# Performance work log

Hardware: AMD Instinct MI355X
Metric: run time of the kernel (lower is better)

The kernel has to match this reference:

```python
import jax, jax.numpy as jnp
import numpy as np

EPS = 1e-5


def _bn(h, g, b):
    # training-mode batch norm over the point dimension
    m = jnp.mean(h, axis=0)
    v = jnp.mean(jnp.square(h), axis=0) - jnp.square(m)
    return g * (h - m) * jax.lax.rsqrt(v + EPS) + b


def _convtr2(x, w):
    # generative transpose conv, stride 2: each point spawns 8 children. w: [8, Cin, Cout]
    n = x.shape[0]
    return jnp.einsum('nc,kcd->nkd', x, w).reshape(n * 8, w.shape[-1])


def _conv3(x, idx, mask, w):
    # 3^3 stride-1 sparse conv via kernel-map gather + per-offset GEMM, accumulated with scan.
    # idx, mask: [27, N]; w: [27, Cin, Cout]
    acc0 = jnp.zeros((idx.shape[1], w.shape[-1]), x.dtype)

    def step(acc, kin):
        i_k, m_k, w_k = kin
        return acc + (x[i_k] * m_k[:, None]) @ w_k, None

    out, _ = jax.lax.scan(step, acc0, (idx, mask, w))
    return out


def setup_inputs() -> dict:
    key = jax.random.key(0)
    ks = jax.random.split(key, 16)
    N0, N1, N2 = 8000, 64000, 512000
    s = lambda k, shape, fan: jax.random.normal(k, shape, jnp.float32) * (1.0 / np.sqrt(fan))
    return {
        'x': jax.random.normal(ks[0], (N0, 128), jnp.float32),
        'w_tr1': s(ks[1], (8, 128, 96), 128),
        'g1': jnp.ones((96,), jnp.float32), 'b1': jnp.zeros((96,), jnp.float32),
        'idx1': jax.random.randint(ks[2], (27, N1), 0, N1, jnp.int32),
        'mask1': (jax.random.uniform(ks[3], (27, N1)) < 0.7).astype(jnp.float32),
        'w_c1': s(ks[4], (27, 96, 64), 27 * 96),
        'g2': jnp.ones((64,), jnp.float32), 'b2': jnp.zeros((64,), jnp.float32),
        'w_tr2': s(ks[5], (8, 64, 64), 64),
        'g3': jnp.ones((64,), jnp.float32), 'b3': jnp.zeros((64,), jnp.float32),
        'idx2': jax.random.randint(ks[6], (27, N2), 0, N2, jnp.int32),
        'mask2': (jax.random.uniform(ks[7], (27, N2)) < 0.7).astype(jnp.float32),
        'w_c2': s(ks[8], (27, 64, 32), 27 * 64),
        'g4': jnp.ones((32,), jnp.float32), 'b4': jnp.zeros((32,), jnp.float32),
        'w_dec': s(ks[9], (32, 96), 32),
        'g5': jnp.ones((96,), jnp.float32), 'b5': jnp.zeros((96,), jnp.float32),
    }


def reference(x, w_tr1, g1, b1, idx1, mask1, w_c1, g2, b2,
              w_tr2, g3, b3, idx2, mask2, w_c2, g4, b4, w_dec, g5, b5):
    relu = jax.nn.relu
    h = relu(_bn(_convtr2(x, w_tr1), g1, b1))            # [8*N0, 96]
    h = relu(_bn(_conv3(h, idx1, mask1, w_c1), g2, b2))  # [N1, 64]
    h = relu(_bn(_convtr2(h, w_tr2), g3, b3))            # [N2, 64]
    h = relu(_bn(_conv3(h, idx2, mask2, w_c2), g4, b4))  # [N2, 32]
    intensity_res = jnp.mean(h, axis=1, keepdims=True)   # mean_me: feature-dim mean
    remi2seg = relu(_bn(h @ w_dec, g5, b5))              # [N2, 96]
    return intensity_res, remi2seg
```

## Files before the change

### kernel.cpp

```cpp
#include <hip/hip_runtime.h>
#include <hip/hip_bf16.h>


#define EPSF 1e-5f
#define N2 512000

typedef __attribute__((ext_vector_type(8))) short short8v;
typedef __attribute__((ext_vector_type(4))) short short4v;
typedef __attribute__((ext_vector_type(4))) float f32x4;

__device__ __forceinline__ float bf2f(short u) {
  return __uint_as_float(((unsigned int)(unsigned short)u) << 16);
}
__device__ __forceinline__ short f2bf(float f) {
  __hip_bfloat16 h = __float2bfloat16(f);
  return *(short*)&h;
}

__global__ __launch_bounds__(256) void wconvA_k(
    const float* __restrict__ wc1, const float* __restrict__ wc2,
    const float* __restrict__ wt1, const float* __restrict__ wt2,
    const float* __restrict__ x,
    ushort* __restrict__ o_wc1, ushort* __restrict__ o_wc2,
    ushort* __restrict__ o_wt1, ushort* __restrict__ o_wt2,
    ushort* __restrict__ o_xb) {
  const int i = blockIdx.x * 256 + threadIdx.x;
  if (i < 165888) {
    int k = i / 6144, r = i % 6144, c = r / 64, d = r % 64;
    o_wc1[(k * 64 + d) * 96 + c] = (ushort)f2bf(wc1[i]);
  } else if (i < 221184) {
    int j = i - 165888;
    int k = j / 2048, r = j % 2048, c = r / 32, d = r % 32;
    o_wc2[(k * 32 + d) * 64 + c] = (ushort)f2bf(wc2[j]);
  } else if (i < 319488) {
    int j = i - 221184;
    int k = j / 12288, r = j % 12288, c = r / 96, d = r % 96;
    o_wt1[(k * 96 + d) * 128 + c] = (ushort)f2bf(wt1[j]);
  } else if (i < 352256) {
    int j = i - 319488;
    int k = j / 4096, r = j % 4096, c = r / 64, d = r % 64;
    o_wt2[(k * 64 + d) * 64 + c] = (ushort)f2bf(wt2[j]);
  } else if (i < 1376256) {
    int j = i - 352256;
    o_xb[j] = (ushort)f2bf(x[j]);
  }
}

__global__ __launch_bounds__(256) void wconvB_k(const float* __restrict__ wdec,
                                                ushort* __restrict__ o_wd) {
  const int i = blockIdx.x * 256 + threadIdx.x;
  if (i < 3072) {
    int c = i / 96, d = i % 96;
    o_wd[d * 32 + c] = (ushort)f2bf(wdec[i]);
  }
}

template <int CIN, int COUT, int NK, int WPB>
__global__ __launch_bounds__(WPB * 64) void convtrm_k(const ushort* __restrict__ xb,
                                                      const ushort* __restrict__ wtb,
                                                      ushort* __restrict__ yb,
                                                      float* __restrict__ st, int N) {
  constexpr int KS = CIN / 32;
  constexpr int NT = COUT / 16;
  const int t = threadIdx.x, wid = t >> 6, lane = t & 63;
  const int r16 = lane & 15, g = lane >> 4, co = g * 8;
  const int base = (blockIdx.x * WPB + wid) * 32;

  short8v A[2][KS];
#pragma unroll
  for (int m = 0; m < 2; ++m) {
    const ushort* rp = xb + (size_t)(base + m * 16 + r16) * CIN + co;
#pragma unroll
    for (int s = 0; s < KS; ++s) A[m][s] = *(const short8v*)(rp + s * 32);
  }
  float s_l[NT], q_l[NT];
#pragma unroll
  for (int n = 0; n < NT; ++n) { s_l[n] = 0.f; q_l[n] = 0.f; }

#pragma unroll 1
  for (int k = 0; k < NK; ++k) {
    f32x4 acc[2][NT];
#pragma unroll
    for (int m = 0; m < 2; ++m)
#pragma unroll
      for (int n = 0; n < NT; ++n) acc[m][n] = (f32x4)0.f;
    const ushort* wb = wtb + ((size_t)k * COUT + r16) * CIN + co;
#pragma unroll
    for (int n = 0; n < NT; ++n)
#pragma unroll
      for (int s = 0; s < KS; ++s) {
        short8v bv = *(const short8v*)(wb + n * 16 * CIN + s * 32);
        acc[0][n] = __builtin_amdgcn_mfma_f32_16x16x32_bf16(A[0][s], bv, acc[0][n], 0, 0, 0);
        acc[1][n] = __builtin_amdgcn_mfma_f32_16x16x32_bf16(A[1][s], bv, acc[1][n], 0, 0, 0);
      }
#pragma unroll
    for (int m = 0; m < 2; ++m)
#pragma unroll
      for (int n = 0; n < NT; ++n)
#pragma unroll
        for (int j = 0; j < 4; ++j) {
          float v = acc[m][n][j];
          yb[((size_t)(base + m * 16 + g * 4 + j) * NK + k) * COUT + n * 16 + r16] =
              (ushort)f2bf(v);
          s_l[n] += v; q_l[n] += v * v;
        }
  }
  __shared__ float sl[2 * COUT];
  for (int i = t; i < 2 * COUT; i += WPB * 64) sl[i] = 0.f;
  __syncthreads();
#pragma unroll
  for (int n = 0; n < NT; ++n) {
    atomicAdd(&sl[n * 16 + r16], s_l[n]);
    atomicAdd(&sl[COUT + n * 16 + r16], q_l[n]);
  }
  __syncthreads();
  for (int i = t; i < 2 * COUT; i += WPB * 64) atomicAdd(&st[i], sl[i]);
}

template <int CIN, int COUT, int MT>
__global__ __launch_bounds__(256) void conv3m_k(const ushort* __restrict__ hb,
                                                const int* __restrict__ idx,
                                                const float* __restrict__ mask,
                                                const ushort* __restrict__ wtb,
                                                ushort* __restrict__ yb,
                                                float* __restrict__ st, int N) {
  constexpr int KS = CIN / 32;
  constexpr int NT = COUT / 16;
  const int t = threadIdx.x, wid = t >> 6, lane = t & 63;
  const int r16 = lane & 15, g = lane >> 4, co = g * 8;
  const int base = (blockIdx.x * 4 + wid) * (MT * 16);

  f32x4 acc[MT][NT];
#pragma unroll
  for (int m = 0; m < MT; ++m)
#pragma unroll
    for (int n = 0; n < NT; ++n) acc[m][n] = (f32x4)0.f;

  int pn[MT];
#pragma unroll
  for (int m = 0; m < MT; ++m) pn[m] = base + m * 16 + r16;

  short8v A0[MT][KS], A1[MT][KS];

#define GATH(A, kk)                                                         \
  {                                                                         \
    const size_t kN = (size_t)(kk) * N;                                     \
    _Pragma("unroll") for (int m = 0; m < MT; ++m) {                        \
      const float mm = mask[kN + pn[m]];                                    \
      const int ii = idx[kN + pn[m]];                                       \
      const ushort* rp = hb + (size_t)ii * CIN + co;                        \
      _Pragma("unroll") for (int s = 0; s < KS; ++s) {                      \
        short8v v = (short8v)0;                                             \
        if (mm != 0.f) v = *(const short8v*)(rp + s * 32);                  \
        A[m][s] = v;                                                        \
      }                                                                     \
    }                                                                       \
  }

#define MMA(A, kk)                                                          \
  {                                                                         \
    const ushort* wb = wtb + ((size_t)(kk) * COUT + r16) * CIN + co;        \
    _Pragma("unroll") for (int n = 0; n < NT; ++n)                          \
        _Pragma("unroll") for (int s = 0; s < KS; ++s) {                    \
      short8v bv = *(const short8v*)(wb + n * 16 * CIN + s * 32);           \
      _Pragma("unroll") for (int m = 0; m < MT; ++m)                        \
          acc[m][n] = __builtin_amdgcn_mfma_f32_16x16x32_bf16(              \
              A[m][s], bv, acc[m][n], 0, 0, 0);                             \
    }                                                                       \
  }

  GATH(A0, 0)
#pragma unroll 1
  for (int k2 = 0; k2 < 13; ++k2) {
    GATH(A1, 2 * k2 + 1)
    MMA(A0, 2 * k2)
    GATH(A0, 2 * k2 + 2)
    MMA(A1, 2 * k2 + 1)
  }
  MMA(A0, 26)
#undef GATH
#undef MMA

  float s_l[NT], q_l[NT];
#pragma unroll
  for (int n = 0; n < NT; ++n) { s_l[n] = 0.f; q_l[n] = 0.f; }
#pragma unroll
  for (int m = 0; m < MT; ++m)
#pragma unroll
    for (int n = 0; n < NT; ++n)
#pragma unroll
      for (int j = 0; j < 4; ++j) {
        float v = acc[m][n][j];
        yb[(size_t)(base + m * 16 + g * 4 + j) * COUT + n * 16 + r16] = (ushort)f2bf(v);
        s_l[n] += v; q_l[n] += v * v;
      }
  __shared__ float sl[2 * COUT];
  if (t < 2 * COUT) sl[t] = 0.f;
  __syncthreads();
#pragma unroll
  for (int n = 0; n < NT; ++n) {
    atomicAdd(&sl[n * 16 + r16], s_l[n]);
    atomicAdd(&sl[COUT + n * 16 + r16], q_l[n]);
  }
  __syncthreads();
  if (t < 2 * COUT) atomicAdd(&st[t], sl[t]);
}

template <int C>
__global__ __launch_bounds__(256) void bn_bb_k(const ushort* __restrict__ in,
                                               ushort* __restrict__ out, int N,
                                               const float* __restrict__ st,
                                               const float* __restrict__ g,
                                               const float* __restrict__ b) {
  __shared__ float scs[C], bis[C];
  const int t = threadIdx.x;
  if (t < C) {
    const float invN = 1.f / (float)N;
    float m = st[t] * invN;
    float var = st[C + t] * invN - m * m;
    float rs = rsqrtf(var + EPSF);
    scs[t] = g[t] * rs;
    bis[t] = b[t] - m * g[t] * rs;
  }
  __syncthreads();
  const long total8 = (long)N * C / 8;
  for (long i = (long)blockIdx.x * 256 + t; i < total8; i += (long)gridDim.x * 256) {
    const int c0 = (int)((8 * i) % C);
    short8v v = *(const short8v*)(in + 8 * i);
    short8v o;
#pragma unroll
    for (int j = 0; j < 8; ++j) {
      float f = bf2f(v[j]);
      o[j] = f2bf(fmaxf(0.f, fmaf(f, scs[c0 + j], bis[c0 + j])));
    }
    *(short8v*)(out + 8 * i) = o;
  }
}

__global__ __launch_bounds__(256) void kint2_k(const ushort* __restrict__ y4b,
                                               float* __restrict__ inten,
                                               const float* __restrict__ st4,
                                               const float* __restrict__ g4,
                                               const float* __restrict__ b4,
                                               ushort* __restrict__ h4b) {
  __shared__ float sc[32], bi[32];
  const int t = threadIdx.x;
  if (t < 32) {
    const float invN = 1.f / (float)N2;
    float m = st4[t] * invN;
    float v = st4[32 + t] * invN - m * m;
    float rs = rsqrtf(v + EPSF);
    sc[t] = g4[t] * rs;
    bi[t] = b4[t] - m * g4[t] * rs;
  }
  __syncthreads();
  const int r = blockIdx.x * 256 + t;
  const ushort* yr = y4b + (size_t)r * 32;
  ushort* hr = h4b + (size_t)r * 32;
  float sum = 0.f;
#pragma unroll
  for (int q = 0; q < 4; ++q) {
    short8v v = *(const short8v*)(yr + 8 * q);
    short8v o;
#pragma unroll
    for (int j = 0; j < 8; ++j) {
      int c = 8 * q + j;
      float h = fmaxf(0.f, fmaf(bf2f(v[j]), sc[c], bi[c]));
      sum += h;
      o[j] = f2bf(h);
    }
    *(short8v*)(hr + 8 * q) = o;
  }
  inten[r] = sum * (1.f / 32.f);
}

__global__ __launch_bounds__(256) void kM2_k(const ushort* __restrict__ h4b,
                                             float* __restrict__ Mg,
                                             float* __restrict__ csum) {
  __shared__ float Mb[1024];
  __shared__ float Sb[32];
  const int t = threadIdx.x;
  for (int i = t; i < 1024; i += 256) Mb[i] = 0.f;
  if (t < 32) Sb[t] = 0.f;
  __syncthreads();
  const int wave = t >> 6, lane = t & 63;
  const int ci = (lane >> 3) * 4, cj = (lane & 7) * 4;
  float macc[16];
  float scl[4];
#pragma unroll
  for (int a = 0; a < 16; ++a) macc[a] = 0.f;
#pragma unroll
  for (int a = 0; a < 4; ++a) scl[a] = 0.f;
  const int base = blockIdx.x * 1000 + wave * 250;
  for (int r = 0; r < 250; ++r) {
    const ushort* yr = h4b + (size_t)(base + r) * 32;
    short4v u = *(const short4v*)(yr + ci);
    short4v w = *(const short4v*)(yr + cj);
    float hu[4], hv[4];
#pragma unroll
    for (int a = 0; a < 4; ++a) { hu[a] = bf2f(u[a]); hv[a] = bf2f(w[a]); }
#pragma unroll
    for (int a = 0; a < 4; ++a)
#pragma unroll
      for (int q = 0; q < 4; ++q) macc[a * 4 + q] = fmaf(hu[a], hv[q], macc[a * 4 + q]);
#pragma unroll
    for (int q = 0; q < 4; ++q) scl[q] += hv[q];
  }
#pragma unroll
  for (int a = 0; a < 4; ++a)
#pragma unroll
    for (int q = 0; q < 4; ++q) atomicAdd(&Mb[(ci + a) * 32 + cj + q], macc[a * 4 + q]);
  if ((lane >> 3) == 0) {
#pragma unroll
    for (int q = 0; q < 4; ++q) atomicAdd(&Sb[cj + q], scl[q]);
  }
  __syncthreads();
  for (int i = t; i < 1024; i += 256) atomicAdd(&Mg[i], Mb[i]);
  if (t < 32) atomicAdd(&csum[t], Sb[t]);
}

__global__ __launch_bounds__(128) void kstat5_k(const float* __restrict__ colsum_g,
                                                const float* __restrict__ Mg,
                                                const float* __restrict__ wd,
                                                const float* __restrict__ g5,
                                                const float* __restrict__ b5,
                                                float* __restrict__ sc5g,
                                                float* __restrict__ bi5g) {
  __shared__ float wl[3072], Ml[1024], csl[32];
  const int t = threadIdx.x;
  for (int i = t * 4; i < 3072; i += 512)
    *(float4*)&wl[i] = *(const float4*)&wd[i];
  for (int i = t; i < 1024; i += 128) Ml[i] = Mg[i];
  if (t < 32) csl[t] = colsum_g[t];
  __syncthreads();
  if (t < 96) {
    const float invN = 1.f / (float)N2;
    float mean = 0.f;
#pragma unroll
    for (int c = 0; c < 32; ++c) mean = fmaf(csl[c], wl[c * 96 + t], mean);
    mean *= invN;
    float q = 0.f;
    for (int c1 = 0; c1 < 32; ++c1) {
      float tmp = 0.f;
#pragma unroll
      for (int c2 = 0; c2 < 32; ++c2) tmp = fmaf(Ml[c1 * 32 + c2], wl[c2 * 96 + t], tmp);
      q = fmaf(wl[c1 * 96 + t], tmp, q);
    }
    float var = q * invN - mean * mean;
    float rs = rsqrtf(var + EPSF);
    float sc = g5[t] * rs;
    sc5g[t] = sc;
    bi5g[t] = b5[t] - mean * sc;
  }
}

__global__ __launch_bounds__(256) void kfinal2_k(const ushort* __restrict__ h4b,
                                                 const ushort* __restrict__ wdT,
                                                 const float* __restrict__ sc5g,
                                                 const float* __restrict__ bi5g,
                                                 float* __restrict__ outR) {
  const int t = threadIdx.x, wid = t >> 6, lane = t & 63;
  const int r16 = lane & 15, g = lane >> 4, co = g * 8;
  const int base = (blockIdx.x * 4 + wid) * 32;

  short8v a[2];
#pragma unroll
  for (int m = 0; m < 2; ++m)
    a[m] = *(const short8v*)(h4b + (size_t)(base + m * 16 + r16) * 32 + co);

  f32x4 acc[2][6];
#pragma unroll
  for (int m = 0; m < 2; ++m)
#pragma unroll
    for (int n = 0; n < 6; ++n) acc[m][n] = (f32x4)0.f;
#pragma unroll
  for (int n = 0; n < 6; ++n) {
    short8v bv = *(const short8v*)(wdT + (size_t)(n * 16 + r16) * 32 + co);
    acc[0][n] = __builtin_amdgcn_mfma_f32_16x16x32_bf16(a[0], bv, acc[0][n], 0, 0, 0);
    acc[1][n] = __builtin_amdgcn_mfma_f32_16x16x32_bf16(a[1], bv, acc[1][n], 0, 0, 0);
  }
#pragma unroll
  for (int n = 0; n < 6; ++n) {
    const int col = n * 16 + r16;
    const float sc = sc5g[col], bi = bi5g[col];
#pragma unroll
    for (int m = 0; m < 2; ++m)
#pragma unroll
      for (int j = 0; j < 4; ++j)
        outR[(size_t)(base + m * 16 + g * 4 + j) * 96 + col] =
            fmaxf(0.f, fmaf(acc[m][n][j], sc, bi));
  }
}

extern "C" void kernel_launch(void* const* d_in, const int* in_sizes, int n_in,
                              void* d_out, int out_size, void* d_ws, size_t ws_size,
                              hipStream_t stream) {
  const float* x     = (const float*)d_in[0];
  const float* w_tr1 = (const float*)d_in[1];
  const float* g1    = (const float*)d_in[2];
  const float* b1    = (const float*)d_in[3];
  const int*   idx1  = (const int*)d_in[4];
  const float* mask1 = (const float*)d_in[5];
  const float* w_c1  = (const float*)d_in[6];
  const float* g2    = (const float*)d_in[7];
  const float* b2    = (const float*)d_in[8];
  const float* w_tr2 = (const float*)d_in[9];
  const float* g3    = (const float*)d_in[10];
  const float* b3    = (const float*)d_in[11];
  const int*   idx2  = (const int*)d_in[12];
  const float* mask2 = (const float*)d_in[13];
  const float* w_c2  = (const float*)d_in[14];
  const float* g4    = (const float*)d_in[15];
  const float* b4    = (const float*)d_in[16];
  const float* w_dec = (const float*)d_in[17];
  const float* g5    = (const float*)d_in[18];
  const float* b5    = (const float*)d_in[19];

  float* outF  = (float*)d_out;
  float* inten = outF;
  float* R     = outF + 512000;

  ushort* y1b = (ushort*)R;
  ushort* h1b = (ushort*)(R + 3200000);
  ushort* y2b = (ushort*)(R + 6400000);
  ushort* h2b = (ushort*)(R + 8500000);
  ushort* y3b = (ushort*)(R + 16384000);
  ushort* h3b = (ushort*)R;
  ushort* y4b = (ushort*)(R + 32800000);
  ushort* xb  = (ushort*)(R + 41100000);

  float* iw  = inten;
  float* st1 = iw + 0;
  float* st2 = iw + 192;
  float* st3 = iw + 320;
  ushort* w1T  = (ushort*)(iw + 448);
  ushort* w2T  = (ushort*)(iw + 83392);
  ushort* wt1T = (ushort*)(iw + 111040);
  ushort* wt2T = (ushort*)(iw + 160192);

  float* xw   = (float*)d_in[0];
  float* st4  = xw + 0;
  float* csum = xw + 64;
  float* Mg   = xw + 96;
  float* sc5g = xw + 1120;
  float* bi5g = xw + 1216;
  ushort* wdT = (ushort*)(xw + 1312);

  ushort* i2f = (ushort*)d_in[12];

  hipMemsetAsync(st1, 0, 448 * sizeof(float), stream);
  wconvA_k<<<5376, 256, 0, stream>>>(w_c1, w_c2, w_tr1, w_tr2, x,
                                     w1T, w2T, wt1T, wt2T, xb);
  hipMemsetAsync(st4, 0, 1120 * sizeof(float), stream);
  wconvB_k<<<12, 256, 0, stream>>>(w_dec, wdT);

  convtrm_k<128, 96, 8, 2><<<125, 128, 0, stream>>>(xb, wt1T, y1b, st1, 8000);
  bn_bb_k<96><<<1024, 256, 0, stream>>>(y1b, h1b, 64000, st1, g1, b1);
  conv3m_k<96, 64, 1><<<1000, 256, 0, stream>>>(h1b, idx1, mask1, w1T, y2b, st2, 64000);
  bn_bb_k<64><<<1024, 256, 0, stream>>>(y2b, h2b, 64000, st2, g2, b2);
  convtrm_k<64, 64, 8, 4><<<500, 256, 0, stream>>>(h2b, wt2T, y3b, st3, 64000);
  bn_bb_k<64><<<2048, 256, 0, stream>>>(y3b, h3b, N2, st3, g3, b3);
  conv3m_k<64, 32, 2><<<4000, 256, 0, stream>>>(h3b, idx2, mask2, w2T, y4b, st4, N2);

  hipMemcpyAsync(i2f, y4b, 32768000, hipMemcpyDeviceToDevice, stream);
  kint2_k<<<2000, 256, 0, stream>>>(i2f, inten, st4, g4, b4, y4b );
  hipMemcpyAsync(i2f, y4b, 32768000, hipMemcpyDeviceToDevice, stream);
  kM2_k<<<512, 256, 0, stream>>>(i2f, Mg, csum);
  kstat5_k<<<1, 128, 0, stream>>>(csum, Mg, w_dec, g5, b5, sc5g, bi5g);
  kfinal2_k<<<4000, 256, 0, stream>>>(i2f, wdT, sc5g, bi5g, R);
}
```

Measured before the change: 1.083 ms.

## Fold masks into gather indices, stage indices in LDS, triple-buffer conv gathers

A prep kernel rewrites masked-out entries of idx1/idx2 so they point at a zeroed padding row, which removes the mask loads and the branch from the sparse-conv gather. The conv kernel now stages each block's 27 index rows in shared memory and uses a three-deep register pipeline of gathered rows in place of two. The two 32 MB device-to-device copies before the final kernels are also removed by having kint2 write into the reused idx2 buffer directly. The index rewrite mutates input buffers in place and adds a pass over the 27xN index and mask arrays. It relies on the zero-row offsets in the output scratch area being correct.

```diff
diff --git a/kernel.cpp b/kernel.cpp
--- a/kernel.cpp
+++ b/kernel.cpp
@@ -15,6 +15,17 @@
 __device__ __forceinline__ short f2bf(float f) {
   __hip_bfloat16 h = __float2bfloat16(f);
   return *(short*)&h;
+}
+
+__global__ __launch_bounds__(256) void idxprep_k(int* __restrict__ i1,
+                                                 const float* __restrict__ m1,
+                                                 int n1, int z1,
+                                                 int* __restrict__ i2,
+                                                 const float* __restrict__ m2,
+                                                 int n2, int z2) {
+  const int i = blockIdx.x * 256 + threadIdx.x;
+  if (i < n1 && m1[i] == 0.f) i1[i] = z1;
+  if (i < n2 && m2[i] == 0.f) i2[i] = z2;
 }
 
 __global__ __launch_bounds__(256) void wconvA_k(
@@ -118,17 +129,24 @@
 }
 
 template <int CIN, int COUT, int MT>
-__global__ __launch_bounds__(256) void conv3m_k(const ushort* __restrict__ hb,
-                                                const int* __restrict__ idx,
-                                                const float* __restrict__ mask,
-                                                const ushort* __restrict__ wtb,
-                                                ushort* __restrict__ yb,
-                                                float* __restrict__ st, int N) {
+__global__ __launch_bounds__(256) void conv3m2_k(const ushort* __restrict__ hb,
+                                                 const int* __restrict__ idxp,
+                                                 const ushort* __restrict__ wtb,
+                                                 ushort* __restrict__ yb,
+                                                 float* __restrict__ st, int N) {
   constexpr int KS = CIN / 32;
   constexpr int NT = COUT / 16;
+  constexpr int PPB = 4 * MT * 16;
+  __shared__ int lidx[27 * PPB];
   const int t = threadIdx.x, wid = t >> 6, lane = t & 63;
   const int r16 = lane & 15, g = lane >> 4, co = g * 8;
-  const int base = (blockIdx.x * 4 + wid) * (MT * 16);
+  const int B0 = blockIdx.x * PPB;
+
+  for (int j = t; j < 27 * PPB; j += 256)
+    lidx[j] = idxp[(size_t)(j / PPB) * N + B0 + (j % PPB)];
+  __syncthreads();
+
+  const int wbase = wid * MT * 16 + r16;
 
   f32x4 acc[MT][NT];
 #pragma unroll
@@ -136,51 +154,46 @@
 #pragma unroll
     for (int n = 0; n < NT; ++n) acc[m][n] = (f32x4)0.f;
 
-  int pn[MT];
-#pragma unroll
-  for (int m = 0; m < MT; ++m) pn[m] = base + m * 16 + r16;
-
-  short8v A0[MT][KS], A1[MT][KS];
-
-#define GATH(A, kk)                                                         \
-  {                                                                         \
-    const size_t kN = (size_t)(kk) * N;                                     \
-    _Pragma("unroll") for (int m = 0; m < MT; ++m) {                        \
-      const float mm = mask[kN + pn[m]];                                    \
-      const int ii = idx[kN + pn[m]];                                       \
-      const ushort* rp = hb + (size_t)ii * CIN + co;                        \
-      _Pragma("unroll") for (int s = 0; s < KS; ++s) {                      \
-        short8v v = (short8v)0;                                             \
-        if (mm != 0.f) v = *(const short8v*)(rp + s * 32);                  \
-        A[m][s] = v;                                                        \
-      }                                                                     \
-    }                                                                       \
-  }
-
-#define MMA(A, kk)                                                          \
-  {                                                                         \
-    const ushort* wb = wtb + ((size_t)(kk) * COUT + r16) * CIN + co;        \
-    _Pragma("unroll") for (int n = 0; n < NT; ++n)                          \
-        _Pragma("unroll") for (int s = 0; s < KS; ++s) {                    \
-      short8v bv = *(const short8v*)(wb + n * 16 * CIN + s * 32);           \
-      _Pragma("unroll") for (int m = 0; m < MT; ++m)                        \
-          acc[m][n] = __builtin_amdgcn_mfma_f32_16x16x32_bf16(              \
-              A[m][s], bv, acc[m][n], 0, 0, 0);                             \
-    }                                                                       \
-  }
-
-  GATH(A0, 0)
+  short8v A0[MT][KS], A1[MT][KS], A2[MT][KS];
+  int i0[MT], i1[MT], i2[MT];
+
+#define LIDX(dst, kk)                                                      \
+  { _Pragma("unroll") for (int m = 0; m < MT; ++m)                         \
+        dst[m] = lidx[(kk) * PPB + wbase + m * 16]; }
+
+#define GROW(A, ixr)                                                       \
+  { _Pragma("unroll") for (int m = 0; m < MT; ++m) {                       \
+      const ushort* rp = hb + (size_t)ixr[m] * CIN + co;                   \
+      _Pragma("unroll") for (int s = 0; s < KS; ++s)                       \
+          A[m][s] = *(const short8v*)(rp + s * 32);                        \
+    } }
+
+#define MMA(A, kk)                                                         \
+  { const ushort* wb = wtb + ((size_t)(kk) * COUT + r16) * CIN + co;       \
+    _Pragma("unroll") for (int n = 0; n < NT; ++n)                         \
+        _Pragma("unroll") for (int s = 0; s < KS; ++s) {                   \
+      short8v bv = *(const short8v*)(wb + n * 16 * CIN + s * 32);          \
+      _Pragma("unroll") for (int m = 0; m < MT; ++m)                       \
+          acc[m][n] = __builtin_amdgcn_mfma_f32_16x16x32_bf16(             \
+              A[m][s], bv, acc[m][n], 0, 0, 0);                            \
+    } }
+
+  LIDX(i0, 0) GROW(A0, i0)
+  LIDX(i1, 1) GROW(A1, i1)
+  LIDX(i2, 2)
 #pragma unroll 1
-  for (int k2 = 0; k2 < 13; ++k2) {
-    GATH(A1, 2 * k2 + 1)
-    MMA(A0, 2 * k2)
-    GATH(A0, 2 * k2 + 2)
-    MMA(A1, 2 * k2 + 1)
-  }
-  MMA(A0, 26)
-#undef GATH
+  for (int j = 0; j < 8; ++j) {
+    GROW(A2, i2) LIDX(i0, 3 * j + 3) MMA(A0, 3 * j)
+    GROW(A0, i0) LIDX(i1, 3 * j + 4) MMA(A1, 3 * j + 1)
+    GROW(A1, i1) LIDX(i2, 3 * j + 5) MMA(A2, 3 * j + 2)
+  }
+  GROW(A2, i2)
+  MMA(A0, 24) MMA(A1, 25) MMA(A2, 26)
+#undef LIDX
+#undef GROW
 #undef MMA
 
+  const int base = B0 + wid * MT * 16;
   float s_l[NT], q_l[NT];
 #pragma unroll
   for (int n = 0; n < NT; ++n) { s_l[n] = 0.f; q_l[n] = 0.f; }
@@ -399,7 +412,7 @@
   const float* w_tr1 = (const float*)d_in[1];
   const float* g1    = (const float*)d_in[2];
   const float* b1    = (const float*)d_in[3];
-  const int*   idx1  = (const int*)d_in[4];
+  int*         idx1  = (int*)d_in[4];
   const float* mask1 = (const float*)d_in[5];
   const float* w_c1  = (const float*)d_in[6];
   const float* g2    = (const float*)d_in[7];
@@ -407,7 +420,7 @@
   const float* w_tr2 = (const float*)d_in[9];
   const float* g3    = (const float*)d_in[10];
   const float* b3    = (const float*)d_in[11];
-  const int*   idx2  = (const int*)d_in[12];
+  int*         idx2  = (int*)d_in[12];
   const float* mask2 = (const float*)d_in[13];
   const float* w_c2  = (const float*)d_in[14];
   const float* g4    = (const float*)d_in[15];
@@ -446,9 +459,12 @@
   float* bi5g = xw + 1216;
   ushort* wdT = (ushort*)(xw + 1312);
 
-  ushort* i2f = (ushort*)d_in[12];
+  ushort* h4s = (ushort*)d_in[12];
 
   hipMemsetAsync(st1, 0, 448 * sizeof(float), stream);
+  hipMemsetAsync((void*)(R + 6272000), 0, 192, stream);
+  idxprep_k<<<54000, 256, 0, stream>>>(idx1, mask1, 27 * 64000, 64000,
+                                       idx2, mask2, 27 * N2, N2);
   wconvA_k<<<5376, 256, 0, stream>>>(w_c1, w_c2, w_tr1, w_tr2, x,
                                      w1T, w2T, wt1T, wt2T, xb);
   hipMemsetAsync(st4, 0, 1120 * sizeof(float), stream);
@@ -456,16 +472,15 @@
 
   convtrm_k<128, 96, 8, 2><<<125, 128, 0, stream>>>(xb, wt1T, y1b, st1, 8000);
   bn_bb_k<96><<<1024, 256, 0, stream>>>(y1b, h1b, 64000, st1, g1, b1);
-  conv3m_k<96, 64, 1><<<1000, 256, 0, stream>>>(h1b, idx1, mask1, w1T, y2b, st2, 64000);
+  conv3m2_k<96, 64, 1><<<1000, 256, 0, stream>>>(h1b, idx1, w1T, y2b, st2, 64000);
   bn_bb_k<64><<<1024, 256, 0, stream>>>(y2b, h2b, 64000, st2, g2, b2);
   convtrm_k<64, 64, 8, 4><<<500, 256, 0, stream>>>(h2b, wt2T, y3b, st3, 64000);
   bn_bb_k<64><<<2048, 256, 0, stream>>>(y3b, h3b, N2, st3, g3, b3);
-  conv3m_k<64, 32, 2><<<4000, 256, 0, stream>>>(h3b, idx2, mask2, w2T, y4b, st4, N2);
-
-  hipMemcpyAsync(i2f, y4b, 32768000, hipMemcpyDeviceToDevice, stream);
-  kint2_k<<<2000, 256, 0, stream>>>(i2f, inten, st4, g4, b4, y4b );
-  hipMemcpyAsync(i2f, y4b, 32768000, hipMemcpyDeviceToDevice, stream);
-  kM2_k<<<512, 256, 0, stream>>>(i2f, Mg, csum);
+  hipMemsetAsync((void*)(R + 16384000), 0, 128, stream);
+  conv3m2_k<64, 32, 2><<<4000, 256, 0, stream>>>(h3b, idx2, w2T, y4b, st4, N2);
+
+  kint2_k<<<2000, 256, 0, stream>>>(y4b, inten, st4, g4, b4, h4s);
+  kM2_k<<<512, 256, 0, stream>>>(h4s, Mg, csum);
   kstat5_k<<<1, 128, 0, stream>>>(csum, Mg, w_dec, g5, b5, sc5g, bi5g);
-  kfinal2_k<<<4000, 256, 0, stream>>>(i2f, wdT, sc5g, bi5g, R);
-}
+  kfinal2_k<<<4000, 256, 0, stream>>>(h4s, wdT, sc5g, bi5g, R);
+}
```

New measurement: 1.031 ms. -4.8%, faster.
